# Performance work log

Measured on AMD Instinct MI355X. Metric: run time of the kernel, lower is better.

Reference implementation:

```python
import jax, jax.numpy as jnp
import numpy as np

INPUT_DIM = 128
BATCH = 4096
N_FORMULAS = 256
N_CONJ_ARR = [6, 9, 12, 15]
DEPTH_ARR = [2, 4, 6]
KEEP_PROB_ARR = [0.1, 0.3, 0.5, 0.7, 0.9]
EPS = 1.0  # binary_threshold_eps


def _build_structure():
    # Formulas split evenly across the 4 conjunction-count groups; each formula's
    # conjunctions split evenly across the 3 depths. Each literal belongs to exactly
    # one conjunction; each conjunction to exactly one formula (block-sparse structure).
    group = N_FORMULAS // len(N_CONJ_ARR)
    f_of_l, c_of_l, f_of_c = [], [], []
    cid = 0
    for f in range(N_FORMULAS):
        nc = N_CONJ_ARR[f // group]
        for d in DEPTH_ARR:
            for _ in range(nc // len(DEPTH_ARR)):
                f_of_c.append(f)
                f_of_l.extend([f] * d)
                c_of_l.extend([cid] * d)
                cid += 1
    return (np.array(f_of_l, np.int32), np.array(c_of_l, np.int32),
            np.array(f_of_c, np.int32))


def setup_inputs() -> dict:
    f_of_l, c_of_l, f_of_c = _build_structure()
    L = f_of_l.shape[0]  # 10752 literals
    rng = np.random.default_rng(0)
    # generate_random_mask: per-formula keep prob cycles through KEEP_PROB_ARR,
    # feature mask is Bernoulli(p) per formula, extended to every literal of that formula.
    p = np.array([KEEP_PROB_ARR[f % len(KEEP_PROB_ARR)] for f in range(N_FORMULAS)])
    formulas_random_mask = (rng.random((INPUT_DIM, N_FORMULAS)) < p).astype(np.float32)
    literals_random_mask = formulas_random_mask[:, f_of_l]  # (D, L)
    fan = INPUT_DIM + L
    glorot = rng.normal(0.0, np.sqrt(2.0 / fan), size=(INPUT_DIM, L)).astype(np.float32)
    key = jax.random.key(0)
    kx, kmu, ksig = jax.random.split(key, 3)
    return {
        "x": jax.random.normal(kx, (BATCH, INPUT_DIM), dtype=jnp.float32),
        # build(): self.weight = glorot_weight * literals_random_mask
        "weight": jnp.asarray(glorot * literals_random_mask),
        "bias": jnp.zeros((L,), jnp.float32),
        # learnable_mask initialized to binary_threshold_eps + 0.5
        "learnable_mask": jnp.full((INPUT_DIM, N_FORMULAS), EPS + 0.5, jnp.float32),
        # keras random_normal initializer default stddev = 0.05
        "mu": 0.05 * jax.random.normal(kmu, (N_FORMULAS, INPUT_DIM), dtype=jnp.float32),
        "sigma": 0.05 * jax.random.normal(ksig, (1, N_FORMULAS, INPUT_DIM), dtype=jnp.float32),
        "temperature": jnp.full((1,), 2.0, jnp.float32),
        "formula_of_literal": jnp.asarray(f_of_l),
        "conj_of_literal": jnp.asarray(c_of_l),
        "formula_of_conj": jnp.asarray(f_of_c),
    }


def reference(x, weight, bias, learnable_mask, mu, sigma, temperature,
              formula_of_literal, conj_of_literal, formula_of_conj):
    L = weight.shape[1]
    n_conj = formula_of_conj.shape[0]
    n_formulas = mu.shape[0]
    dt = weight.dtype

    # FeatureSelection: binary threshold + extension-matrix sparse matmul (gather form)
    mask01 = (jnp.abs(learnable_mask) > EPS).astype(dt)          # (D, F)
    learnable_binary_mask = mask01[:, formula_of_literal]        # (D, L) == M01 @ ext_matrix

    # and/or biases = column sums of the 0/1 indicator matrices
    and_bias = jax.ops.segment_sum(jnp.ones((L,), dt), conj_of_literal, num_segments=n_conj)
    or_bias = jax.ops.segment_sum(jnp.ones((n_conj,), dt), formula_of_conj, num_segments=n_formulas)

    # literals: tanh(x @ (W * M) + b)
    out_literals = jnp.tanh(x @ (weight * learnable_binary_mask) + bias)  # (B, L)

    # sparse indicator matmuls as segment sums over the literal/conjunction axis
    conj_sum = jax.ops.segment_sum(out_literals.T, conj_of_literal, num_segments=n_conj).T  # (B, C)
    out_conjunctions = jnp.tanh(conj_sum - and_bias + 1.5)       # soft AND
    form_sum = jax.ops.segment_sum(out_conjunctions.T, formula_of_conj, num_segments=n_formulas).T
    out_dnnfs = jnp.tanh(form_sum + or_bias - 1.5)               # soft OR, (B, F)

    # Localization: RBF distance -> sigmoid(temperature)-scaled softmax
    diff = x[:, None, :] - mu[None, :, :]                        # (B, F, D)
    loc = jnp.exp(-jnp.linalg.norm(diff * sigma, axis=-1))       # (B, F)
    loc = jax.nn.softmax(jax.nn.sigmoid(temperature) * loc, axis=-1)

    return out_dnnfs * loc
```

## Files before the change

### kernel.cpp

```cpp
#include <hip/hip_runtime.h>

#define L_TOT 10752
#define NF    256
#define BATCHN 4096

typedef __attribute__((ext_vector_type(8))) short short8;
typedef __attribute__((ext_vector_type(4))) float f32x4;

__device__ __forceinline__ unsigned short f2bf(float f) {
  unsigned int u = __float_as_uint(f);
  unsigned int r = (u + 0x7FFFu + ((u >> 16) & 1u)) >> 16;
  return (unsigned short)r;
}

__device__ __forceinline__ float tanh_fast(float x) {
  float e2 = __builtin_amdgcn_exp2f(x * 2.8853900817779268f);
  float r  = __builtin_amdgcn_rcpf(e2 + 1.0f);
  return fmaf(-2.0f, r, 1.0f);
}

template<int G> struct Sch;
template<> struct Sch<0> {
  static constexpr int NT = 2, NC = 6;
  static constexpr int p6[2]  = {0b11, 0};
  static constexpr int m4[2]  = {0, 0b0011};
  static constexpr int m2a[2] = {0, 0b0100};
  static constexpr int m2b[2] = {0, 0b0100};
};
template<> struct Sch<1> {
  static constexpr int NT = 3, NC = 9;
  static constexpr int p6[3]  = {0b11, 0b01, 0};
  static constexpr int m4[3]  = {0, 0b1100, 0b0001};
  static constexpr int m2a[3] = {0, 0, 0b0110};
  static constexpr int m2b[3] = {0, 0, 0b0010};
};
template<> struct Sch<2> {
  static constexpr int NT = 4, NC = 12;
  static constexpr int p6[4]  = {0b11, 0b11, 0, 0};
  static constexpr int m4[4]  = {0, 0, 0b1111, 0};
  static constexpr int m2a[4] = {0, 0, 0, 0b0011};
  static constexpr int m2b[4] = {0, 0, 0, 0b0011};
};
template<> struct Sch<3> {
  static constexpr int NT = 5, NC = 15;
  static constexpr int p6[5]  = {0b11, 0b11, 0b01, 0, 0};
  static constexpr int m4[5]  = {0, 0, 0b1100, 0b0111, 0};
  static constexpr int m2a[5] = {0, 0, 0, 0b1000, 0b0011};
  static constexpr int m2b[5] = {0, 0, 0, 0b1000, 0b0001};
};

template<int G>
__device__ __forceinline__ void prep_w_body(
    const float* __restrict__ weight, const float* __restrict__ bias,
    const float* __restrict__ lm, int f, int ls, int fbase,
    unsigned short* __restrict__ WT, float* __restrict__ bias_p,
    unsigned short* s_t)
{
  using S = Sch<G>;
  constexpr int n3 = S::NC / 3;
  constexpr int LF = 12 * n3;
  constexpr int NROWS = S::NT * 16;
  const int tid = threadIdx.x;
  for (int e = tid; e < 128 * LF; e += 256) {
    int k = e / LF;
    int j = e - k * LF;
    float m = (fabsf(lm[k * NF + f]) > 1.0f) ? 1.0f : 0.0f;
    s_t[j * 136 + k] = f2bf(weight[(size_t)k * L_TOT + ls + j] * m);
  }
  __syncthreads();
  const int k = tid & 127, rb = tid >> 7;
  for (int R = rb; R < NROWS; R += 2) {
    int j = -1;
    if (R < 8 * n3)        { int dd = R & 7; if (dd < 6) j = 6 * n3 + 6 * (R >> 3) + dd; }
    else if (R < 12 * n3)  j = R - 6 * n3;
    else if (R < 14 * n3)  j = R - 12 * n3;
    unsigned short v = (j >= 0) ? s_t[j * 136 + k] : (unsigned short)0;
    WT[(size_t)(fbase + R) * 128 + k] = v;
    if (k == 0) bias_p[fbase + R] = (j >= 0) ? bias[ls + j] : 0.0f;
  }
}

__global__ __launch_bounds__(256) void prep_all(
    const float4* __restrict__ x4, ushort4* __restrict__ a2,
    const float* __restrict__ mu, const float* __restrict__ sigma,
    unsigned short* __restrict__ B2, float* __restrict__ cf,
    const float* __restrict__ weight, const float* __restrict__ bias,
    const float* __restrict__ lm,
    unsigned short* __restrict__ WT, float* __restrict__ bias_p)
{
  __shared__ unsigned short s_t[60 * 136];
  int bi = blockIdx.x, tid = threadIdx.x;
  if (bi < 512) {
    int i = bi * 256 + tid;
    float4 v = x4[i];
    int b = i >> 5, kc = i & 31;
    ushort4 sq, xx;
    sq.x = f2bf(v.x * v.x); sq.y = f2bf(v.y * v.y);
    sq.z = f2bf(v.z * v.z); sq.w = f2bf(v.w * v.w);
    xx.x = f2bf(v.x); xx.y = f2bf(v.y); xx.z = f2bf(v.z); xx.w = f2bf(v.w);
    a2[b * 64 + kc] = sq;
    a2[b * 64 + 32 + kc] = xx;
  } else if (bi < 576) {
    int f = (bi - 512) * 4 + (tid >> 6);
    int k = tid & 63;
    float acc = 0.0f;
    for (int kk = k; kk < 128; kk += 64) {
      float s = sigma[f * 128 + kk], m = mu[f * 128 + kk];
      float s2 = s * s;
      B2[f * 256 + kk] = f2bf(s2);
      B2[f * 256 + 128 + kk] = f2bf(-2.0f * m * s2);
      acc = fmaf(m * m, s2, acc);
    }
    for (int o = 1; o < 64; o <<= 1) acc += __shfl_xor(acc, o);
    if (k == 0) cf[f] = acc;
  } else {
    int f = bi - 576, g = f >> 6, fo = f & 63;
    if (g == 0)      prep_w_body<0>(weight, bias, lm, f, 0    + fo * 24, fo * 32,        WT, bias_p, s_t);
    else if (g == 1) prep_w_body<1>(weight, bias, lm, f, 1536 + fo * 36, 2048 + fo * 48, WT, bias_p, s_t);
    else if (g == 2) prep_w_body<2>(weight, bias, lm, f, 3840 + fo * 48, 5120 + fo * 64, WT, bias_p, s_t);
    else             prep_w_body<3>(weight, bias, lm, f, 6912 + fo * 60, 9216 + fo * 80, WT, bias_p, s_t);
  }
}

__device__ __forceinline__ short8 ldsw(const unsigned short* s_w, int row, int colb) {
  int off = (row << 8) + (colb ^ ((row & 7) << 4));
  return *reinterpret_cast<const short8*>(reinterpret_cast<const char*>(s_w) + off);
}

template<int G>
__device__ __forceinline__ void dnnf_body(
    const unsigned short* __restrict__ A2,
    const unsigned short* __restrict__ WT,
    const float* __restrict__ bias_p,
    float* __restrict__ dnnf,
    int f, int fbase, int batch0,
    unsigned short* s_w)
{
  using S = Sch<G>;
  constexpr int NT = S::NT;
  const int tid = threadIdx.x;
  const int lane = tid & 63;
  const int wv = tid >> 6;
  const int n = lane & 15;
  const int q = lane >> 4;

  const char* wsrc = reinterpret_cast<const char*>(WT + (size_t)fbase * 128);
#pragma unroll
  for (int p = 0; p < NT; ++p) {
    int c = p * 256 + tid;
    int row = c >> 4;
    int lin = c << 4;
    int swz = lin ^ ((row & 7) << 4);
    uint4 v = *reinterpret_cast<const uint4*>(wsrc + lin);
    *reinterpret_cast<uint4*>(reinterpret_cast<char*>(s_w) + swz) = v;
  }

  f32x4 brg[NT];
#pragma unroll
  for (int t = 0; t < NT; ++t)
    brg[t] = *reinterpret_cast<const f32x4*>(&bias_p[fbase + t * 16 + q * 4]);

  __syncthreads();

  const unsigned short* xr0 = A2 + (size_t)(batch0 + wv * 16 + n) * 256 + 128;
  short8 xc[4], xn[4];
#pragma unroll
  for (int kk = 0; kk < 4; ++kk)
    xc[kk] = *reinterpret_cast<const short8*>(xr0 + kk * 32 + q * 8);

#pragma unroll
  for (int iter = 0; iter < 8; ++iter) {
    if (iter < 7) {
      const unsigned short* xr = xr0 + (size_t)(iter + 1) * 64 * 256;
#pragma unroll
      for (int kk = 0; kk < 4; ++kk)
        xn[kk] = *reinterpret_cast<const short8*>(xr + kk * 32 + q * 8);
    }
    int brow = batch0 + iter * 64 + wv * 16;

    f32x4 acc[NT];
#pragma unroll
    for (int t = 0; t < NT; ++t) acc[t] = (f32x4){0.f, 0.f, 0.f, 0.f};
#pragma unroll
    for (int kk = 0; kk < 4; ++kk)
#pragma unroll
      for (int t = 0; t < NT; ++t)
        acc[t] = __builtin_amdgcn_mfma_f32_16x16x32_bf16(
            ldsw(s_w, t * 16 + n, kk * 64 + q * 16), xc[kk], acc[t], 0, 0, 0);

    float fs = 0.0f;
#pragma unroll
    for (int t = 0; t < NT; ++t) {
      float v0 = tanh_fast(acc[t][0] + brg[t][0]);
      float v1 = tanh_fast(acc[t][1] + brg[t][1]);
      float v2 = tanh_fast(acc[t][2] + brg[t][2]);
      float v3 = tanh_fast(acc[t][3] + brg[t][3]);
      float s = v0 + v1 + v2 + v3;
      if (S::p6[t]) {
        float po = __shfl_xor(s, 16);
        float t6 = tanh_fast(s + po - 4.5f);
        bool add = ((q & 1) == 0) && ((S::p6[t] >> (q >> 1)) & 1);
        fs += add ? t6 : 0.0f;
      }
      if (S::m4[t]) {
        float t4 = tanh_fast(s - 2.5f);
        fs += ((S::m4[t] >> q) & 1) ? t4 : 0.0f;
      }
      if (S::m2a[t]) {
        float ta = tanh_fast(v0 + v1 - 0.5f);
        fs += ((S::m2a[t] >> q) & 1) ? ta : 0.0f;
      }
      if (S::m2b[t]) {
        float tb = tanh_fast(v2 + v3 - 0.5f);
        fs += ((S::m2b[t] >> q) & 1) ? tb : 0.0f;
      }
    }
    fs += __shfl_xor(fs, 16);
    fs += __shfl_xor(fs, 32);
    float dv = tanh_fast(fs + (float)S::NC - 1.5f);
    if (lane < 16)
      dnnf[(size_t)f * BATCHN + brow + n] = dv;

    if (iter < 7) {
#pragma unroll
      for (int kk = 0; kk < 4; ++kk) xc[kk] = xn[kk];
    }
  }
}

__global__ __launch_bounds__(256, 2) void dnnf_main(
    const unsigned short* __restrict__ A2,
    const unsigned short* __restrict__ WT,
    const float* __restrict__ bias_p,
    float* __restrict__ dnnf)
{
  __shared__ __align__(16) unsigned short s_w[80 * 128];
  int bi = blockIdx.x;
  int f = bi >> 3;
  int batch0 = (bi & 7) * 512;
  int g = f >> 6, fo = f & 63;
  if (g == 0)      dnnf_body<0>(A2, WT, bias_p, dnnf, f, fo * 32,        batch0, s_w);
  else if (g == 1) dnnf_body<1>(A2, WT, bias_p, dnnf, f, 2048 + fo * 48, batch0, s_w);
  else if (g == 2) dnnf_body<2>(A2, WT, bias_p, dnnf, f, 5120 + fo * 64, batch0, s_w);
  else             dnnf_body<3>(A2, WT, bias_p, dnnf, f, 9216 + fo * 80, batch0, s_w);
}

__global__ __launch_bounds__(512) void loc_fused(
    const unsigned short* __restrict__ A2,
    const unsigned short* __restrict__ B2,
    const float* __restrict__ cf,
    const float* __restrict__ temp,
    const float* __restrict__ dnnf,
    float* __restrict__ out)
{
  __shared__ float s_part[8][16];
  int tid = threadIdx.x, lane = tid & 63, w = tid >> 6, n = lane & 15, q = lane >> 4;
  int b0 = blockIdx.x * 16;

  const unsigned short* arow = A2 + (size_t)(b0 + n) * 256;
  f32x4 acc[2];
#pragma unroll
  for (int t = 0; t < 2; ++t) acc[t] = (f32x4){0.f, 0.f, 0.f, 0.f};
#pragma unroll
  for (int kk = 0; kk < 8; ++kk) {
    short8 af = *reinterpret_cast<const short8*>(arow + kk * 32 + q * 8);
#pragma unroll
    for (int t = 0; t < 2; ++t) {
      const unsigned short* brow = B2 + (size_t)(w * 32 + t * 16 + n) * 256;
      short8 bf = *reinterpret_cast<const short8*>(brow + kk * 32 + q * 8);
      acc[t] = __builtin_amdgcn_mfma_f32_16x16x32_bf16(af, bf, acc[t], 0, 0, 0);
    }
  }

  float T = temp[0];
  float sg = 1.0f / (1.0f + __builtin_amdgcn_exp2f(-T * 1.4426950408889634f));
  float ez[2][4];
  float sr[4] = {0.f, 0.f, 0.f, 0.f};
#pragma unroll
  for (int t = 0; t < 2; ++t) {
    float c = cf[w * 32 + t * 16 + n];
#pragma unroll
    for (int r = 0; r < 4; ++r) {
      float n2 = fmaxf(acc[t][r] + c, 0.0f);
      float loc = __builtin_amdgcn_exp2f(-__builtin_amdgcn_sqrtf(n2) * 1.4426950408889634f);
      float e = __builtin_amdgcn_exp2f(sg * loc * 1.4426950408889634f);
      ez[t][r] = e;
      sr[r] += e;
    }
  }
#pragma unroll
  for (int o = 1; o < 16; o <<= 1)
#pragma unroll
    for (int r = 0; r < 4; ++r) sr[r] += __shfl_xor(sr[r], o);
  if (n == 0) {
#pragma unroll
    for (int r = 0; r < 4; ++r) s_part[w][q * 4 + r] = sr[r];
  }
  __syncthreads();
  float rtot[4];
#pragma unroll
  for (int r = 0; r < 4; ++r) {
    float tot = 0.0f;
#pragma unroll
    for (int ww = 0; ww < 8; ++ww) tot += s_part[ww][q * 4 + r];
    rtot[r] = 1.0f / tot;
  }
#pragma unroll
  for (int t = 0; t < 2; ++t) {
    int fc = w * 32 + t * 16 + n;
#pragma unroll
    for (int r = 0; r < 4; ++r) {
      int bg = b0 + q * 4 + r;
      out[(size_t)bg * 256 + fc] = dnnf[(size_t)fc * BATCHN + bg] * ez[t][r] * rtot[r];
    }
  }
}

extern "C" void kernel_launch(void* const* d_in, const int* in_sizes, int n_in,
                              void* d_out, int out_size, void* d_ws, size_t ws_size,
                              hipStream_t stream) {
  const float* x      = (const float*)d_in[0];
  const float* weight = (const float*)d_in[1];
  const float* bias   = (const float*)d_in[2];
  const float* lm     = (const float*)d_in[3];
  const float* mu     = (const float*)d_in[4];
  const float* sigma  = (const float*)d_in[5];
  const float* temp   = (const float*)d_in[6];
  float* out = (float*)d_out;

  char* ws = (char*)d_ws;
  unsigned short* A2     = (unsigned short*)(ws);
  float*          dnnf   = (float*)(ws + 2097152);
  unsigned short* B2     = (unsigned short*)(ws + 6291456);
  float*          cf     = (float*)(ws + 6422528);
  unsigned short* WT     = (unsigned short*)(ws + 6423552);
  float*          bias_p = (float*)(ws + 10093568);

  prep_all<<<832, 256, 0, stream>>>((const float4*)x, (ushort4*)A2,
                                    mu, sigma, B2, cf,
                                    weight, bias, lm, WT, bias_p);
  dnnf_main<<<2048, 256, 0, stream>>>(A2, WT, bias_p, dnnf);
  loc_fused<<<256, 512, 0, stream>>>(A2, B2, cf, temp, dnnf, out);
}
```

Measured before the change: 140.8 us.

## Fuse weight masking/packing into dnnf kernel and double-buffer MFMA tiles

Removes the separate weight-prep stage that wrote a packed, masked bf16 weight matrix to workspace. Each dnnf block now reads the fp32 weights, applies the learnable mask, converts to bf16 and writes them straight into swizzled LDS, with bias kept in LDS. This drops a global round trip but repeats the prep in each of the 8 batch-chunk blocks per formula. The main loop is also double-buffered so the next tile's MFMAs overlap the current tile's tanh reduction. Blocks are remapped to interleave formula groups for load balance, and loc_fused now uses 1024 threads with one tile per wave.

```diff
diff --git a/kernel.cpp b/kernel.cpp
--- a/kernel.cpp
+++ b/kernel.cpp
@@ -49,46 +49,11 @@
   static constexpr int m2b[5] = {0, 0, 0, 0b1000, 0b0001};
 };
 
-template<int G>
-__device__ __forceinline__ void prep_w_body(
-    const float* __restrict__ weight, const float* __restrict__ bias,
-    const float* __restrict__ lm, int f, int ls, int fbase,
-    unsigned short* __restrict__ WT, float* __restrict__ bias_p,
-    unsigned short* s_t)
-{
-  using S = Sch<G>;
-  constexpr int n3 = S::NC / 3;
-  constexpr int LF = 12 * n3;
-  constexpr int NROWS = S::NT * 16;
-  const int tid = threadIdx.x;
-  for (int e = tid; e < 128 * LF; e += 256) {
-    int k = e / LF;
-    int j = e - k * LF;
-    float m = (fabsf(lm[k * NF + f]) > 1.0f) ? 1.0f : 0.0f;
-    s_t[j * 136 + k] = f2bf(weight[(size_t)k * L_TOT + ls + j] * m);
-  }
-  __syncthreads();
-  const int k = tid & 127, rb = tid >> 7;
-  for (int R = rb; R < NROWS; R += 2) {
-    int j = -1;
-    if (R < 8 * n3)        { int dd = R & 7; if (dd < 6) j = 6 * n3 + 6 * (R >> 3) + dd; }
-    else if (R < 12 * n3)  j = R - 6 * n3;
-    else if (R < 14 * n3)  j = R - 12 * n3;
-    unsigned short v = (j >= 0) ? s_t[j * 136 + k] : (unsigned short)0;
-    WT[(size_t)(fbase + R) * 128 + k] = v;
-    if (k == 0) bias_p[fbase + R] = (j >= 0) ? bias[ls + j] : 0.0f;
-  }
-}
-
-__global__ __launch_bounds__(256) void prep_all(
+__global__ __launch_bounds__(256) void prep_xb(
     const float4* __restrict__ x4, ushort4* __restrict__ a2,
     const float* __restrict__ mu, const float* __restrict__ sigma,
-    unsigned short* __restrict__ B2, float* __restrict__ cf,
-    const float* __restrict__ weight, const float* __restrict__ bias,
-    const float* __restrict__ lm,
-    unsigned short* __restrict__ WT, float* __restrict__ bias_p)
-{
-  __shared__ unsigned short s_t[60 * 136];
+    unsigned short* __restrict__ B2, float* __restrict__ cf)
+{
   int bi = blockIdx.x, tid = threadIdx.x;
   if (bi < 512) {
     int i = bi * 256 + tid;
@@ -100,7 +65,7 @@
     xx.x = f2bf(v.x); xx.y = f2bf(v.y); xx.z = f2bf(v.z); xx.w = f2bf(v.w);
     a2[b * 64 + kc] = sq;
     a2[b * 64 + 32 + kc] = xx;
-  } else if (bi < 576) {
+  } else {
     int f = (bi - 512) * 4 + (tid >> 6);
     int k = tid & 63;
     float acc = 0.0f;
@@ -113,12 +78,6 @@
     }
     for (int o = 1; o < 64; o <<= 1) acc += __shfl_xor(acc, o);
     if (k == 0) cf[f] = acc;
-  } else {
-    int f = bi - 576, g = f >> 6, fo = f & 63;
-    if (g == 0)      prep_w_body<0>(weight, bias, lm, f, 0    + fo * 24, fo * 32,        WT, bias_p, s_t);
-    else if (g == 1) prep_w_body<1>(weight, bias, lm, f, 1536 + fo * 36, 2048 + fo * 48, WT, bias_p, s_t);
-    else if (g == 2) prep_w_body<2>(weight, bias, lm, f, 3840 + fo * 48, 5120 + fo * 64, WT, bias_p, s_t);
-    else             prep_w_body<3>(weight, bias, lm, f, 6912 + fo * 60, 9216 + fo * 80, WT, bias_p, s_t);
   }
 }
 
@@ -128,124 +87,152 @@
 }
 
 template<int G>
+__device__ __forceinline__ void mfma_tile(const unsigned short* s_w,
+                                          const short8* xc, f32x4* ac,
+                                          int n, int q)
+{
+  constexpr int NT = Sch<G>::NT;
+#pragma unroll
+  for (int t = 0; t < NT; ++t) ac[t] = (f32x4){0.f, 0.f, 0.f, 0.f};
+#pragma unroll
+  for (int kk = 0; kk < 4; ++kk)
+#pragma unroll
+    for (int t = 0; t < NT; ++t)
+      ac[t] = __builtin_amdgcn_mfma_f32_16x16x32_bf16(
+          ldsw(s_w, t * 16 + n, kk * 64 + q * 16), xc[kk], ac[t], 0, 0, 0);
+}
+
+template<int G>
+__device__ __forceinline__ void reduce_store(const f32x4* ac, const float* s_bias,
+                                             float* __restrict__ dnnf,
+                                             int f, int brow, int n, int q, int lane)
+{
+  using S = Sch<G>;
+  float fs = 0.0f;
+#pragma unroll
+  for (int t = 0; t < S::NT; ++t) {
+    f32x4 brg = *reinterpret_cast<const f32x4*>(&s_bias[t * 16 + q * 4]);
+    float v0 = tanh_fast(ac[t][0] + brg[0]);
+    float v1 = tanh_fast(ac[t][1] + brg[1]);
+    float v2 = tanh_fast(ac[t][2] + brg[2]);
+    float v3 = tanh_fast(ac[t][3] + brg[3]);
+    float s = v0 + v1 + v2 + v3;
+    if (S::p6[t]) {
+      float po = __shfl_xor(s, 16);
+      float t6 = tanh_fast(s + po - 4.5f);
+      bool add = ((q & 1) == 0) && ((S::p6[t] >> (q >> 1)) & 1);
+      fs += add ? t6 : 0.0f;
+    }
+    if (S::m4[t]) {
+      float t4 = tanh_fast(s - 2.5f);
+      fs += ((S::m4[t] >> q) & 1) ? t4 : 0.0f;
+    }
+    if (S::m2a[t]) {
+      float ta = tanh_fast(v0 + v1 - 0.5f);
+      fs += ((S::m2a[t] >> q) & 1) ? ta : 0.0f;
+    }
+    if (S::m2b[t]) {
+      float tb = tanh_fast(v2 + v3 - 0.5f);
+      fs += ((S::m2b[t] >> q) & 1) ? tb : 0.0f;
+    }
+  }
+  fs += __shfl_xor(fs, 16);
+  fs += __shfl_xor(fs, 32);
+  float dv = tanh_fast(fs + (float)S::NC - 1.5f);
+  if (lane < 16)
+    dnnf[(size_t)f * BATCHN + brow + n] = dv;
+}
+
+template<int G>
 __device__ __forceinline__ void dnnf_body(
     const unsigned short* __restrict__ A2,
-    const unsigned short* __restrict__ WT,
-    const float* __restrict__ bias_p,
+    const float* __restrict__ weight,
+    const float* __restrict__ bias,
+    const float* __restrict__ lm,
     float* __restrict__ dnnf,
-    int f, int fbase, int batch0,
-    unsigned short* s_w)
+    int f, int ls, int batch0,
+    unsigned short* s_w, float* s_bias)
 {
   using S = Sch<G>;
   constexpr int NT = S::NT;
+  constexpr int n3 = S::NC / 3;
+  constexpr int LF = 12 * n3;
   const int tid = threadIdx.x;
   const int lane = tid & 63;
   const int wv = tid >> 6;
   const int n = lane & 15;
   const int q = lane >> 4;
 
-  const char* wsrc = reinterpret_cast<const char*>(WT + (size_t)fbase * 128);
-#pragma unroll
-  for (int p = 0; p < NT; ++p) {
-    int c = p * 256 + tid;
-    int row = c >> 4;
-    int lin = c << 4;
-    int swz = lin ^ ((row & 7) << 4);
-    uint4 v = *reinterpret_cast<const uint4*>(wsrc + lin);
-    *reinterpret_cast<uint4*>(reinterpret_cast<char*>(s_w) + swz) = v;
-  }
-
-  f32x4 brg[NT];
-#pragma unroll
-  for (int t = 0; t < NT; ++t)
-    brg[t] = *reinterpret_cast<const f32x4*>(&bias_p[fbase + t * 16 + q * 4]);
-
+  {
+    unsigned long long* p = reinterpret_cast<unsigned long long*>(s_w);
+    constexpr int n64 = NT * 512;
+#pragma unroll
+    for (int i = tid; i < n64; i += 256) p[i] = 0ull;
+    if (tid < NT * 16) s_bias[tid] = 0.0f;
+  }
   __syncthreads();
+  for (int e = tid; e < 128 * LF; e += 256) {
+    int k = e / LF;
+    int j = e - k * LF;
+    float m = (fabsf(lm[k * NF + f]) > 1.0f) ? 1.0f : 0.0f;
+    unsigned short w = f2bf(weight[(size_t)k * L_TOT + ls + j] * m);
+    int R;
+    if (j < 2 * n3)      R = j + 12 * n3;
+    else if (j < 6 * n3) R = j + 6 * n3;
+    else { unsigned u = (unsigned)(j - 6 * n3); unsigned c = u / 6u;
+           R = 8 * (int)c + (int)(u - 6u * c); }
+    s_w[(R << 7) + (k ^ ((R & 7) << 3))] = w;
+    if (e < LF) s_bias[R] = bias[ls + j];
+  }
+  __syncthreads();
 
   const unsigned short* xr0 = A2 + (size_t)(batch0 + wv * 16 + n) * 256 + 128;
-  short8 xc[4], xn[4];
+  short8 xb[2][4];
+  f32x4 ac[2][NT];
 #pragma unroll
   for (int kk = 0; kk < 4; ++kk)
-    xc[kk] = *reinterpret_cast<const short8*>(xr0 + kk * 32 + q * 8);
-
-#pragma unroll
-  for (int iter = 0; iter < 8; ++iter) {
-    if (iter < 7) {
-      const unsigned short* xr = xr0 + (size_t)(iter + 1) * 64 * 256;
+    xb[0][kk] = *reinterpret_cast<const short8*>(xr0 + kk * 32 + q * 8);
+  mfma_tile<G>(s_w, xb[0], ac[0], n, q);
+#pragma unroll
+  for (int kk = 0; kk < 4; ++kk)
+    xb[1][kk] = *reinterpret_cast<const short8*>(xr0 + 64 * 256 + kk * 32 + q * 8);
+
+#pragma unroll
+  for (int i = 0; i < 8; ++i) {
+    const int cur = i & 1, nxt = cur ^ 1;
+    if (i + 2 < 8) {
+      const unsigned short* xr = xr0 + (size_t)(i + 2) * 64 * 256;
 #pragma unroll
       for (int kk = 0; kk < 4; ++kk)
-        xn[kk] = *reinterpret_cast<const short8*>(xr + kk * 32 + q * 8);
-    }
-    int brow = batch0 + iter * 64 + wv * 16;
-
-    f32x4 acc[NT];
-#pragma unroll
-    for (int t = 0; t < NT; ++t) acc[t] = (f32x4){0.f, 0.f, 0.f, 0.f};
-#pragma unroll
-    for (int kk = 0; kk < 4; ++kk)
-#pragma unroll
-      for (int t = 0; t < NT; ++t)
-        acc[t] = __builtin_amdgcn_mfma_f32_16x16x32_bf16(
-            ldsw(s_w, t * 16 + n, kk * 64 + q * 16), xc[kk], acc[t], 0, 0, 0);
-
-    float fs = 0.0f;
-#pragma unroll
-    for (int t = 0; t < NT; ++t) {
-      float v0 = tanh_fast(acc[t][0] + brg[t][0]);
-      float v1 = tanh_fast(acc[t][1] + brg[t][1]);
-      float v2 = tanh_fast(acc[t][2] + brg[t][2]);
-      float v3 = tanh_fast(acc[t][3] + brg[t][3]);
-      float s = v0 + v1 + v2 + v3;
-      if (S::p6[t]) {
-        float po = __shfl_xor(s, 16);
-        float t6 = tanh_fast(s + po - 4.5f);
-        bool add = ((q & 1) == 0) && ((S::p6[t] >> (q >> 1)) & 1);
-        fs += add ? t6 : 0.0f;
-      }
-      if (S::m4[t]) {
-        float t4 = tanh_fast(s - 2.5f);
-        fs += ((S::m4[t] >> q) & 1) ? t4 : 0.0f;
-      }
-      if (S::m2a[t]) {
-        float ta = tanh_fast(v0 + v1 - 0.5f);
-        fs += ((S::m2a[t] >> q) & 1) ? ta : 0.0f;
-      }
-      if (S::m2b[t]) {
-        float tb = tanh_fast(v2 + v3 - 0.5f);
-        fs += ((S::m2b[t] >> q) & 1) ? tb : 0.0f;
-      }
-    }
-    fs += __shfl_xor(fs, 16);
-    fs += __shfl_xor(fs, 32);
-    float dv = tanh_fast(fs + (float)S::NC - 1.5f);
-    if (lane < 16)
-      dnnf[(size_t)f * BATCHN + brow + n] = dv;
-
-    if (iter < 7) {
-#pragma unroll
-      for (int kk = 0; kk < 4; ++kk) xc[kk] = xn[kk];
-    }
+        xb[cur][kk] = *reinterpret_cast<const short8*>(xr + kk * 32 + q * 8);
+    }
+    if (i + 1 < 8)
+      mfma_tile<G>(s_w, xb[nxt], ac[nxt], n, q);
+    reduce_store<G>(ac[cur], s_bias, dnnf, f, batch0 + i * 64 + wv * 16, n, q, lane);
   }
 }
 
 __global__ __launch_bounds__(256, 2) void dnnf_main(
     const unsigned short* __restrict__ A2,
-    const unsigned short* __restrict__ WT,
-    const float* __restrict__ bias_p,
+    const float* __restrict__ weight,
+    const float* __restrict__ bias,
+    const float* __restrict__ lm,
     float* __restrict__ dnnf)
 {
   __shared__ __align__(16) unsigned short s_w[80 * 128];
+  __shared__ __align__(16) float s_bias[80];
   int bi = blockIdx.x;
-  int f = bi >> 3;
+  int u = bi >> 3;
+  int f = ((u & 3) << 6) | (u >> 2);
   int batch0 = (bi & 7) * 512;
-  int g = f >> 6, fo = f & 63;
-  if (g == 0)      dnnf_body<0>(A2, WT, bias_p, dnnf, f, fo * 32,        batch0, s_w);
-  else if (g == 1) dnnf_body<1>(A2, WT, bias_p, dnnf, f, 2048 + fo * 48, batch0, s_w);
-  else if (g == 2) dnnf_body<2>(A2, WT, bias_p, dnnf, f, 5120 + fo * 64, batch0, s_w);
-  else             dnnf_body<3>(A2, WT, bias_p, dnnf, f, 9216 + fo * 80, batch0, s_w);
-}
-
-__global__ __launch_bounds__(512) void loc_fused(
+  int g = u & 3, fo = u >> 2;
+  if (g == 0)      dnnf_body<0>(A2, weight, bias, lm, dnnf, f, 0    + fo * 24, batch0, s_w, s_bias);
+  else if (g == 1) dnnf_body<1>(A2, weight, bias, lm, dnnf, f, 1536 + fo * 36, batch0, s_w, s_bias);
+  else if (g == 2) dnnf_body<2>(A2, weight, bias, lm, dnnf, f, 3840 + fo * 48, batch0, s_w, s_bias);
+  else             dnnf_body<3>(A2, weight, bias, lm, dnnf, f, 6912 + fo * 60, batch0, s_w, s_bias);
+}
+
+__global__ __launch_bounds__(1024) void loc_fused(
     const unsigned short* __restrict__ A2,
     const unsigned short* __restrict__ B2,
     const float* __restrict__ cf,
@@ -253,40 +240,32 @@
     const float* __restrict__ dnnf,
     float* __restrict__ out)
 {
-  __shared__ float s_part[8][16];
+  __shared__ float s_part[16][16];
   int tid = threadIdx.x, lane = tid & 63, w = tid >> 6, n = lane & 15, q = lane >> 4;
   int b0 = blockIdx.x * 16;
 
   const unsigned short* arow = A2 + (size_t)(b0 + n) * 256;
-  f32x4 acc[2];
-#pragma unroll
-  for (int t = 0; t < 2; ++t) acc[t] = (f32x4){0.f, 0.f, 0.f, 0.f};
+  const unsigned short* brow = B2 + (size_t)(w * 16 + n) * 256;
+  f32x4 acc = (f32x4){0.f, 0.f, 0.f, 0.f};
 #pragma unroll
   for (int kk = 0; kk < 8; ++kk) {
     short8 af = *reinterpret_cast<const short8*>(arow + kk * 32 + q * 8);
-#pragma unroll
-    for (int t = 0; t < 2; ++t) {
-      const unsigned short* brow = B2 + (size_t)(w * 32 + t * 16 + n) * 256;
-      short8 bf = *reinterpret_cast<const short8*>(brow + kk * 32 + q * 8);
-      acc[t] = __builtin_amdgcn_mfma_f32_16x16x32_bf16(af, bf, acc[t], 0, 0, 0);
-    }
+    short8 bf = *reinterpret_cast<const short8*>(brow + kk * 32 + q * 8);
+    acc = __builtin_amdgcn_mfma_f32_16x16x32_bf16(af, bf, acc, 0, 0, 0);
   }
 
   float T = temp[0];
   float sg = 1.0f / (1.0f + __builtin_amdgcn_exp2f(-T * 1.4426950408889634f));
-  float ez[2][4];
-  float sr[4] = {0.f, 0.f, 0.f, 0.f};
-#pragma unroll
-  for (int t = 0; t < 2; ++t) {
-    float c = cf[w * 32 + t * 16 + n];
-#pragma unroll
-    for (int r = 0; r < 4; ++r) {
-      float n2 = fmaxf(acc[t][r] + c, 0.0f);
-      float loc = __builtin_amdgcn_exp2f(-__builtin_amdgcn_sqrtf(n2) * 1.4426950408889634f);
-      float e = __builtin_amdgcn_exp2f(sg * loc * 1.4426950408889634f);
-      ez[t][r] = e;
-      sr[r] += e;
-    }
+  float ez[4];
+  float sr[4];
+  float c = cf[w * 16 + n];
+#pragma unroll
+  for (int r = 0; r < 4; ++r) {
+    float n2 = fmaxf(acc[r] + c, 0.0f);
+    float loc = __builtin_amdgcn_exp2f(-__builtin_amdgcn_sqrtf(n2) * 1.4426950408889634f);
+    float e = __builtin_amdgcn_exp2f(sg * loc * 1.4426950408889634f);
+    ez[r] = e;
+    sr[r] = e;
   }
 #pragma unroll
   for (int o = 1; o < 16; o <<= 1)
@@ -302,17 +281,14 @@
   for (int r = 0; r < 4; ++r) {
     float tot = 0.0f;
 #pragma unroll
-    for (int ww = 0; ww < 8; ++ww) tot += s_part[ww][q * 4 + r];
+    for (int ww = 0; ww < 16; ++ww) tot += s_part[ww][q * 4 + r];
     rtot[r] = 1.0f / tot;
   }
 #pragma unroll
-  for (int t = 0; t < 2; ++t) {
-    int fc = w * 32 + t * 16 + n;
-#pragma unroll
-    for (int r = 0; r < 4; ++r) {
-      int bg = b0 + q * 4 + r;
-      out[(size_t)bg * 256 + fc] = dnnf[(size_t)fc * BATCHN + bg] * ez[t][r] * rtot[r];
-    }
+  for (int r = 0; r < 4; ++r) {
+    int fc = w * 16 + n;
+    int bg = b0 + q * 4 + r;
+    out[(size_t)bg * 256 + fc] = dnnf[(size_t)fc * BATCHN + bg] * ez[r] * rtot[r];
   }
 }
 
@@ -333,12 +309,9 @@
   float*          dnnf   = (float*)(ws + 2097152);
   unsigned short* B2     = (unsigned short*)(ws + 6291456);
   float*          cf     = (float*)(ws + 6422528);
-  unsigned short* WT     = (unsigned short*)(ws + 6423552);
-  float*          bias_p = (float*)(ws + 10093568);
-
-  prep_all<<<832, 256, 0, stream>>>((const float4*)x, (ushort4*)A2,
-                                    mu, sigma, B2, cf,
-                                    weight, bias, lm, WT, bias_p);
-  dnnf_main<<<2048, 256, 0, stream>>>(A2, WT, bias_p, dnnf);
-  loc_fused<<<256, 512, 0, stream>>>(A2, B2, cf, temp, dnnf, out);
-}
+
+  prep_xb<<<576, 256, 0, stream>>>((const float4*)x, (ushort4*)A2,
+                                   mu, sigma, B2, cf);
+  dnnf_main<<<2048, 256, 0, stream>>>(A2, weight, bias, lm, dnnf);
+  loc_fused<<<256, 1024, 0, stream>>>(A2, B2, cf, temp, dnnf, out);
+}
```

Result: slower. 173.9 us (+23.5%).

## Cut register pressure in dnnf kernel, interleave formula groups, widen loc kernel

Applied to the files above, without the earlier changes.

The dnnf kernel no longer software-prefetches the next x tile and no longer keeps all accumulators and biases live. It now computes one tile at a time and loads the bias per tile, so it can run at a higher occupancy (launch bounds raised to 8 blocks per CU). Block-to-formula mapping now interleaves the four conjunction-count groups to balance work across CUs. The loc kernel uses 1024 threads with one 16-column tile per wave instead of two. The trade is lost explicit load/compute overlap in exchange for more concurrent waves.

```diff
diff --git a/kernel.cpp b/kernel.cpp
--- a/kernel.cpp
+++ b/kernel.cpp
@@ -154,47 +154,32 @@
     uint4 v = *reinterpret_cast<const uint4*>(wsrc + lin);
     *reinterpret_cast<uint4*>(reinterpret_cast<char*>(s_w) + swz) = v;
   }
-
-  f32x4 brg[NT];
-#pragma unroll
-  for (int t = 0; t < NT; ++t)
-    brg[t] = *reinterpret_cast<const f32x4*>(&bias_p[fbase + t * 16 + q * 4]);
-
   __syncthreads();
 
   const unsigned short* xr0 = A2 + (size_t)(batch0 + wv * 16 + n) * 256 + 128;
-  short8 xc[4], xn[4];
-#pragma unroll
-  for (int kk = 0; kk < 4; ++kk)
-    xc[kk] = *reinterpret_cast<const short8*>(xr0 + kk * 32 + q * 8);
+  const float* bp = bias_p + fbase + q * 4;
 
 #pragma unroll
   for (int iter = 0; iter < 8; ++iter) {
-    if (iter < 7) {
-      const unsigned short* xr = xr0 + (size_t)(iter + 1) * 64 * 256;
+    const unsigned short* xr = xr0 + (size_t)iter * 64 * 256;
+    short8 xc[4];
+#pragma unroll
+    for (int kk = 0; kk < 4; ++kk)
+      xc[kk] = *reinterpret_cast<const short8*>(xr + kk * 32 + q * 8);
+
+    float fs = 0.0f;
+#pragma unroll
+    for (int t = 0; t < NT; ++t) {
+      f32x4 acc = (f32x4){0.f, 0.f, 0.f, 0.f};
 #pragma unroll
       for (int kk = 0; kk < 4; ++kk)
-        xn[kk] = *reinterpret_cast<const short8*>(xr + kk * 32 + q * 8);
-    }
-    int brow = batch0 + iter * 64 + wv * 16;
-
-    f32x4 acc[NT];
-#pragma unroll
-    for (int t = 0; t < NT; ++t) acc[t] = (f32x4){0.f, 0.f, 0.f, 0.f};
-#pragma unroll
-    for (int kk = 0; kk < 4; ++kk)
-#pragma unroll
-      for (int t = 0; t < NT; ++t)
-        acc[t] = __builtin_amdgcn_mfma_f32_16x16x32_bf16(
-            ldsw(s_w, t * 16 + n, kk * 64 + q * 16), xc[kk], acc[t], 0, 0, 0);
-
-    float fs = 0.0f;
-#pragma unroll
-    for (int t = 0; t < NT; ++t) {
-      float v0 = tanh_fast(acc[t][0] + brg[t][0]);
-      float v1 = tanh_fast(acc[t][1] + brg[t][1]);
-      float v2 = tanh_fast(acc[t][2] + brg[t][2]);
-      float v3 = tanh_fast(acc[t][3] + brg[t][3]);
+        acc = __builtin_amdgcn_mfma_f32_16x16x32_bf16(
+            ldsw(s_w, t * 16 + n, kk * 64 + q * 16), xc[kk], acc, 0, 0, 0);
+      f32x4 brg = *reinterpret_cast<const f32x4*>(bp + t * 16);
+      float v0 = tanh_fast(acc[0] + brg[0]);
+      float v1 = tanh_fast(acc[1] + brg[1]);
+      float v2 = tanh_fast(acc[2] + brg[2]);
+      float v3 = tanh_fast(acc[3] + brg[3]);
       float s = v0 + v1 + v2 + v3;
       if (S::p6[t]) {
         float po = __shfl_xor(s, 16);
@@ -219,16 +204,11 @@
     fs += __shfl_xor(fs, 32);
     float dv = tanh_fast(fs + (float)S::NC - 1.5f);
     if (lane < 16)
-      dnnf[(size_t)f * BATCHN + brow + n] = dv;
-
-    if (iter < 7) {
-#pragma unroll
-      for (int kk = 0; kk < 4; ++kk) xc[kk] = xn[kk];
-    }
-  }
-}
-
-__global__ __launch_bounds__(256, 2) void dnnf_main(
+      dnnf[(size_t)f * BATCHN + batch0 + iter * 64 + wv * 16 + n] = dv;
+  }
+}
+
+__global__ __launch_bounds__(256, 8) void dnnf_main(
     const unsigned short* __restrict__ A2,
     const unsigned short* __restrict__ WT,
     const float* __restrict__ bias_p,
@@ -236,16 +216,17 @@
 {
   __shared__ __align__(16) unsigned short s_w[80 * 128];
   int bi = blockIdx.x;
-  int f = bi >> 3;
+  int u = bi >> 3;
   int batch0 = (bi & 7) * 512;
-  int g = f >> 6, fo = f & 63;
+  int g = u & 3, fo = u >> 2;
+  int f = (g << 6) | fo;
   if (g == 0)      dnnf_body<0>(A2, WT, bias_p, dnnf, f, fo * 32,        batch0, s_w);
   else if (g == 1) dnnf_body<1>(A2, WT, bias_p, dnnf, f, 2048 + fo * 48, batch0, s_w);
   else if (g == 2) dnnf_body<2>(A2, WT, bias_p, dnnf, f, 5120 + fo * 64, batch0, s_w);
   else             dnnf_body<3>(A2, WT, bias_p, dnnf, f, 9216 + fo * 80, batch0, s_w);
 }
 
-__global__ __launch_bounds__(512) void loc_fused(
+__global__ __launch_bounds__(1024) void loc_fused(
     const unsigned short* __restrict__ A2,
     const unsigned short* __restrict__ B2,
     const float* __restrict__ cf,
@@ -253,40 +234,32 @@
     const float* __restrict__ dnnf,
     float* __restrict__ out)
 {
-  __shared__ float s_part[8][16];
+  __shared__ float s_part[16][16];
   int tid = threadIdx.x, lane = tid & 63, w = tid >> 6, n = lane & 15, q = lane >> 4;
   int b0 = blockIdx.x * 16;
 
   const unsigned short* arow = A2 + (size_t)(b0 + n) * 256;
-  f32x4 acc[2];
-#pragma unroll
-  for (int t = 0; t < 2; ++t) acc[t] = (f32x4){0.f, 0.f, 0.f, 0.f};
+  const unsigned short* brow = B2 + (size_t)(w * 16 + n) * 256;
+  f32x4 acc = (f32x4){0.f, 0.f, 0.f, 0.f};
 #pragma unroll
   for (int kk = 0; kk < 8; ++kk) {
     short8 af = *reinterpret_cast<const short8*>(arow + kk * 32 + q * 8);
-#pragma unroll
-    for (int t = 0; t < 2; ++t) {
-      const unsigned short* brow = B2 + (size_t)(w * 32 + t * 16 + n) * 256;
-      short8 bf = *reinterpret_cast<const short8*>(brow + kk * 32 + q * 8);
-      acc[t] = __builtin_amdgcn_mfma_f32_16x16x32_bf16(af, bf, acc[t], 0, 0, 0);
-    }
+    short8 bf = *reinterpret_cast<const short8*>(brow + kk * 32 + q * 8);
+    acc = __builtin_amdgcn_mfma_f32_16x16x32_bf16(af, bf, acc, 0, 0, 0);
   }
 
   float T = temp[0];
   float sg = 1.0f / (1.0f + __builtin_amdgcn_exp2f(-T * 1.4426950408889634f));
-  float ez[2][4];
-  float sr[4] = {0.f, 0.f, 0.f, 0.f};
-#pragma unroll
-  for (int t = 0; t < 2; ++t) {
-    float c = cf[w * 32 + t * 16 + n];
-#pragma unroll
-    for (int r = 0; r < 4; ++r) {
-      float n2 = fmaxf(acc[t][r] + c, 0.0f);
-      float loc = __builtin_amdgcn_exp2f(-__builtin_amdgcn_sqrtf(n2) * 1.4426950408889634f);
-      float e = __builtin_amdgcn_exp2f(sg * loc * 1.4426950408889634f);
-      ez[t][r] = e;
-      sr[r] += e;
-    }
+  float ez[4];
+  float sr[4];
+  float c = cf[w * 16 + n];
+#pragma unroll
+  for (int r = 0; r < 4; ++r) {
+    float n2 = fmaxf(acc[r] + c, 0.0f);
+    float loc = __builtin_amdgcn_exp2f(-__builtin_amdgcn_sqrtf(n2) * 1.4426950408889634f);
+    float e = __builtin_amdgcn_exp2f(sg * loc * 1.4426950408889634f);
+    ez[r] = e;
+    sr[r] = e;
   }
 #pragma unroll
   for (int o = 1; o < 16; o <<= 1)
@@ -302,17 +275,14 @@
   for (int r = 0; r < 4; ++r) {
     float tot = 0.0f;
 #pragma unroll
-    for (int ww = 0; ww < 8; ++ww) tot += s_part[ww][q * 4 + r];
+    for (int ww = 0; ww < 16; ++ww) tot += s_part[ww][q * 4 + r];
     rtot[r] = 1.0f / tot;
   }
 #pragma unroll
-  for (int t = 0; t < 2; ++t) {
-    int fc = w * 32 + t * 16 + n;
-#pragma unroll
-    for (int r = 0; r < 4; ++r) {
-      int bg = b0 + q * 4 + r;
-      out[(size_t)bg * 256 + fc] = dnnf[(size_t)fc * BATCHN + bg] * ez[t][r] * rtot[r];
-    }
+  for (int r = 0; r < 4; ++r) {
+    int fc = w * 16 + n;
+    int bg = b0 + q * 4 + r;
+    out[(size_t)bg * 256 + fc] = dnnf[(size_t)fc * BATCHN + bg] * ez[r] * rtot[r];
   }
 }
 
@@ -340,5 +310,5 @@
                                     mu, sigma, B2, cf,
                                     weight, bias, lm, WT, bias_p);
   dnnf_main<<<2048, 256, 0, stream>>>(A2, WT, bias_p, dnnf);
-  loc_fused<<<256, 512, 0, stream>>>(A2, B2, cf, temp, dnnf, out);
-}
+  loc_fused<<<256, 1024, 0, stream>>>(A2, B2, cf, temp, dnnf, out);
+}
```

Result: slower. 265.3 us (+88.4%).
